# Kernel optimization log

Measured on AMD Instinct MI355X. Metric: run time of the kernel, lower is better.

## Reference

```python
import jax, jax.numpy as jnp
import numpy as np

B, S, DM = 2, 2048, 2048
H, DH = 16, 128
EPS = 1e-6


def rmsnorm(t, w):
    # normalize over last dim (head_dim), fp32 math
    var = jnp.mean(jnp.square(t), axis=-1, keepdims=True)
    return t * jax.lax.rsqrt(var + EPS) * w


def apply_rope(t, freqs):
    # t: (B,S,H,D); freqs: (S,1,D/2,2,2)
    b, s, h, d = t.shape
    t2 = t.reshape(b, s, h, 2, d // 2)
    t2 = jnp.moveaxis(t2, -2, -1)[..., None, :]  # (B,S,H,D/2,1,2)
    out = freqs[..., 0] * t2[..., 0] + freqs[..., 1] * t2[..., 1]  # (B,S,H,D/2,2)
    out = jnp.moveaxis(out, -1, -2).reshape(b, s, h, d)
    return out.astype(t.dtype)


def setup_inputs() -> dict:
    key = jax.random.key(0)
    ks = jax.random.split(key, 6)
    sc = 0.02
    return {
        "x": jax.random.normal(ks[0], (B, S, DM), jnp.float32),
        "rope_emb": jax.random.normal(ks[1], (S, 1, DH // 2, 2, 2), jnp.float32),
        "wq": jax.random.normal(ks[2], (DM, DM), jnp.float32) * sc,
        "wk": jax.random.normal(ks[3], (DM, DM), jnp.float32) * sc,
        "wv": jax.random.normal(ks[4], (DM, DM), jnp.float32) * sc,
        "wo": jax.random.normal(ks[5], (DM, DM), jnp.float32) * sc,
        "q_norm_w": jnp.ones((DH,), jnp.float32),
        "k_norm_w": jnp.ones((DH,), jnp.float32),
    }


def reference(x, rope_emb, wq, wk, wv, wo, q_norm_w, k_norm_w):
    b, s, _ = x.shape
    q = (x @ wq.T).reshape(b, s, H, DH)
    k = (x @ wk.T).reshape(b, s, H, DH)
    v = (x @ wv.T).reshape(b, s, H, DH)
    q = rmsnorm(q, q_norm_w)
    k = rmsnorm(k, k_norm_w)
    q = apply_rope(q, rope_emb)
    k = apply_rope(k, rope_emb)
    scale = 1.0 / np.sqrt(DH).astype(np.float32)
    scores = jnp.einsum('bqhd,bkhd->bhqk', q, k) * scale
    attn = jax.nn.softmax(scores, axis=-1)
    out = jnp.einsum('bhqk,bkhd->bqhd', attn, v).reshape(b, s, H * DH)
    return out @ wo.T
```

## Files before the change

kernel.cpp:

```cpp
#include <hip/hip_runtime.h>

typedef __bf16 bf16x8 __attribute__((ext_vector_type(8)));
typedef __bf16 bf16x4 __attribute__((ext_vector_type(4)));
typedef float floatx4 __attribute__((ext_vector_type(4)));

#define GK 2048
#define S_LEN 2048
#define NH 16
#define DH 128
#define NKT (GK / 64)

__device__ __forceinline__ void gl2lds16c(const __bf16* g, char* l) {
    __builtin_amdgcn_global_load_lds(
        (const __attribute__((address_space(1))) void*)g,
        (__attribute__((address_space(3))) void*)l, 16, 0, 0);
}

__global__ __launch_bounds__(256) void cvt_bf16(const float* __restrict__ in,
                                                __bf16* __restrict__ out, int n4) {
    int i = blockIdx.x * 256 + threadIdx.x;
    if (i < n4) {
        const float4 v = ((const float4*)in)[i];
        bf16x4 h;
        h[0] = (__bf16)v.x; h[1] = (__bf16)v.y; h[2] = (__bf16)v.z; h[3] = (__bf16)v.w;
        ((bf16x4*)out)[i] = h;
    }
}

__global__ __launch_bounds__(256) void cvt3_bf16(const float* __restrict__ a,
                                                 const float* __restrict__ b,
                                                 const float* __restrict__ c,
                                                 __bf16* __restrict__ out) {
    const int per = 2048 * 2048 / 4;
    int i = blockIdx.x * 256 + threadIdx.x;
    const float* src = a; int j = i;
    if (i >= 2 * per)      { src = c; j = i - 2 * per; }
    else if (i >= per)     { src = b; j = i - per; }
    const float4 v = ((const float4*)src)[j];
    bf16x4 h;
    h[0] = (__bf16)v.x; h[1] = (__bf16)v.y; h[2] = (__bf16)v.z; h[3] = (__bf16)v.w;
    ((bf16x4*)out)[i] = h;
}

__device__ __forceinline__ int xcd_remap(int L, int nwg) {
    return (L & 7) * (nwg >> 3) + (L >> 3);
}

__device__ __forceinline__ void gemm_body3(const __bf16* __restrict__ A,
                                           const __bf16* __restrict__ W,
                                           int m0, int n0, char* lds,
                                           floatx4 (*acc)[4]) {
    const int t = threadIdx.x, l = t & 63, wave = t >> 6;
    const int fr = l & 15, fq = l >> 4;
    const int wm = wave >> 2, wn = wave & 3;

    const int swcol = ((l & 7) * 8) ^ (((l >> 3) & 7) * 8);
    const __bf16* gA = A + (size_t)(m0 + wave * 8 + (l >> 3)) * GK + swcol;
    const __bf16* gW = W + (size_t)(n0 + wave * 8 + (l >> 3)) * GK + swcol;
    char* const ldsW = lds + wave * 1024;

    auto stageA = [&](int p, int kt, int q) {
        gl2lds16c(gA + (size_t)q * 64 * GK + kt * 64,
                  ldsW + p * 65536 + q * 8192);
    };
    auto stageBh = [&](int p, int kt, int h) {
        gl2lds16c(gW + (size_t)h * 64 * GK + kt * 64,
                  ldsW + p * 65536 + 32768 + h * 8192);
    };

#pragma unroll
    for (int q = 0; q < 4; q++) stageA(0, 0, q);
#pragma unroll
    for (int h = 0; h < 4; h++) stageBh(0, 0, h);
#pragma unroll
    for (int q = 0; q < 4; q++) stageA(1, 1, q);
#pragma unroll
    for (int h = 0; h < 4; h++) stageBh(1, 1, h);

    const int sw = (fr & 7) << 4;
    const int cb0 = (fq * 16) ^ sw;
    const int cb1 = (64 + fq * 16) ^ sw;

    for (int t0 = 0; t0 < NKT; t0++) {
        const int p = t0 & 1;
        if (t0 == NKT - 1) { asm volatile("s_waitcnt vmcnt(0)" ::: "memory"); }
        else               { asm volatile("s_waitcnt vmcnt(8)" ::: "memory"); }
        __builtin_amdgcn_s_barrier();
        asm volatile("" ::: "memory");

        const char* bufA = lds + p * 65536;
        const char* bufB = bufA + 32768;

        bf16x8 bB[4][2];
#pragma unroll
        for (int j = 0; j < 4; j++) {
            const char* rb = bufB + (wn * 64 + j * 16 + fr) * 128;
            bB[j][0] = *(const bf16x8*)(rb + cb0);
            bB[j][1] = *(const bf16x8*)(rb + cb1);
        }

#pragma unroll
        for (int q = 0; q < 4; q++) {
            if (t0 + 2 < NKT) {
                if (q == 1) { stageA(p, t0 + 2, 0); stageBh(p, t0 + 2, 0); stageBh(p, t0 + 2, 1); }
                if (q == 2) { stageA(p, t0 + 2, 1); stageBh(p, t0 + 2, 2); stageBh(p, t0 + 2, 3); }
                if (q == 3) { stageA(p, t0 + 2, 2); }
            }
            const char* ra = bufA + (q * 64 + wm * 32 + fr) * 128;
            bf16x8 bA[2][2];
#pragma unroll
            for (int i = 0; i < 2; i++) {
                bA[i][0] = *(const bf16x8*)(ra + i * 2048 + cb0);
                bA[i][1] = *(const bf16x8*)(ra + i * 2048 + cb1);
            }
            __builtin_amdgcn_s_setprio(1);
#pragma unroll
            for (int i = 0; i < 2; i++)
#pragma unroll
                for (int j = 0; j < 4; j++) {
                    acc[2 * q + i][j] = __builtin_amdgcn_mfma_f32_16x16x32_bf16(bA[i][0], bB[j][0], acc[2 * q + i][j], 0, 0, 0);
                    acc[2 * q + i][j] = __builtin_amdgcn_mfma_f32_16x16x32_bf16(bA[i][1], bB[j][1], acc[2 * q + i][j], 0, 0, 0);
                }
            __builtin_amdgcn_s_setprio(0);
            __builtin_amdgcn_s_barrier();
            asm volatile("" ::: "memory");
        }
        if (t0 + 2 < NKT) stageA(p, t0 + 2, 3);
    }
}

__global__ __launch_bounds__(512, 2) void gemm_qkv(const __bf16* __restrict__ A,
                                                   const __bf16* __restrict__ W,
                                                   __bf16* __restrict__ qb,
                                                   __bf16* __restrict__ kb,
                                                   __bf16* __restrict__ vbT) {
    extern __shared__ __align__(16) char lds[];
    const int gx = gridDim.x;
    const int L = blockIdx.x + gx * blockIdx.y;
    const int tid2 = xcd_remap(L, gx * (int)gridDim.y);
    const int m0 = (tid2 / gx) * 256, n0 = (tid2 % gx) * 256;
    floatx4 acc[8][4] = {};
    gemm_body3(A, W, m0, n0, lds, acc);

    const int lane = threadIdx.x & 63, wave = threadIdx.x >> 6;
    const int fr = lane & 15, fq = lane >> 4;
    const int wm = wave >> 2, wn = wave & 3;
    const int which = n0 >> 11;
    const int nc0 = n0 & 2047;

    for (int mi = 0; mi < 8; mi++)
        for (int j = 0; j < 4; j++) {
            const int row = m0 + (mi >> 1) * 64 + wm * 32 + (mi & 1) * 16 + fq * 4;
            const int col = nc0 + wn * 64 + j * 16 + fr;
            if (which == 2) {
                __bf16* Cp = vbT + (((size_t)(row & ~2047)) << 11) +
                             (size_t)col * 2048 + (row & 2047);
                bf16x4 hv;
                for (int r = 0; r < 4; r++) hv[r] = (__bf16)acc[mi][j][r];
                *(bf16x4*)Cp = hv;
            } else {
                __bf16* dst = which ? kb : qb;
                for (int r = 0; r < 4; r++)
                    dst[(size_t)(row + r) * 2048 + col] = (__bf16)acc[mi][j][r];
            }
        }
}

__global__ __launch_bounds__(512, 2) void gemm_out(const __bf16* __restrict__ A,
                                                   const __bf16* __restrict__ W,
                                                   float* __restrict__ C) {
    extern __shared__ __align__(16) char lds[];
    const int gx = gridDim.x;
    const int L = blockIdx.x + gx * blockIdx.y;
    const int tid2 = xcd_remap(L, gx * (int)gridDim.y);
    const int m0 = (tid2 / gx) * 256, n0 = (tid2 % gx) * 256;
    floatx4 acc[8][4] = {};
    gemm_body3(A, W, m0, n0, lds, acc);

    const int lane = threadIdx.x & 63, wave = threadIdx.x >> 6;
    const int fr = lane & 15, fq = lane >> 4;
    const int wm = wave >> 2, wn = wave & 3;
    for (int mi = 0; mi < 8; mi++)
        for (int j = 0; j < 4; j++) {
            const int row = m0 + (mi >> 1) * 64 + wm * 32 + (mi & 1) * 16 + fq * 4;
            const int col = n0 + wn * 64 + j * 16 + fr;
            for (int r = 0; r < 4; r++)
                C[(size_t)(row + r) * 2048 + col] = acc[mi][j][r];
        }
}

__global__ __launch_bounds__(256) void rmsrope(__bf16* __restrict__ qb,
                                               __bf16* __restrict__ kb,
                                               const float* __restrict__ rope,
                                               const float* __restrict__ qw,
                                               const float* __restrict__ kw) {
    const int lane = threadIdx.x & 63;
    const int row = blockIdx.x * 4 + (threadIdx.x >> 6);
    __bf16* p = (blockIdx.y ? kb : qb) + (size_t)row * DH;
    const float* w = blockIdx.y ? kw : qw;
    const int s = (row >> 4) & (S_LEN - 1);

    float t0 = (float)p[lane];
    float t1 = (float)p[lane + 64];
    float ss = t0 * t0 + t1 * t1;
    for (int o = 32; o; o >>= 1) ss += __shfl_xor(ss, o, 64);
    const float inv = rsqrtf(ss * (1.0f / 128.0f) + 1e-6f);
    t0 *= inv * w[lane];
    t1 *= inv * w[lane + 64];

    const float4 f = *(const float4*)(rope + (size_t)s * 256 + lane * 4);
    p[lane]      = (__bf16)(f.x * t0 + f.y * t1);
    p[lane + 64] = (__bf16)(f.z * t0 + f.w * t1);
}

__global__ __launch_bounds__(256) void flash(const __bf16* __restrict__ Q,
                                             const __bf16* __restrict__ K,
                                             const __bf16* __restrict__ Vt_g,
                                             __bf16* __restrict__ O) {
    __shared__ __align__(16) __bf16 Ks[32][136];
    __shared__ __align__(16) __bf16 Vt[144][40];
    __shared__ __align__(16) __bf16 Ps[4][32][40];

    const int t = threadIdx.x, lane = t & 63, wave = t >> 6;
    const int fr = lane & 15, fq = lane >> 4;

    const int n = blockIdx.x + (int)gridDim.x * blockIdx.y;
    const int by = (n & 7) * 4 + (n >> 7);
    const int bx = (n >> 3) & 15;
    const int b = by >> 4, h = by & 15;

    const size_t baseQ = (size_t)b * S_LEN * 2048 + h * 128;
    const size_t baseV = (size_t)b * 2048 * 2048 + (size_t)h * 128 * 2048;
    const int q0 = bx * 128 + wave * 32;
    const float sc2 = 0.08838834764831845f * 1.4426950408889634f;
    const float M2 = 12.0f * 1.4426950408889634f;

    for (int idx = t; idx < 16 * 40; idx += 256) {
        const int rr = idx / 40, cc = idx - rr * 40;
        Vt[128 + rr][cc] = (rr == 0) ? (__bf16)1.0f : (__bf16)0.0f;
    }

    bf16x8 qf[2][4];
    for (int i2 = 0; i2 < 2; i2++) {
        const __bf16* qp = Q + baseQ + (size_t)(q0 + i2 * 16 + fr) * 2048 + fq * 8;
        for (int c = 0; c < 4; c++) qf[i2][c] = *(const bf16x8*)(qp + c * 32);
    }

    floatx4 oa[2][9] = {};

    const __bf16* Kp = K + baseQ + (size_t)(t >> 3) * 2048 + (t & 7) * 16;
    const __bf16* Vp = Vt_g + baseV + (size_t)(t >> 1) * 2048 + (t & 1) * 16;

    for (int kv0 = 0; kv0 < S_LEN; kv0 += 32) {
        *(uint4*)&Ks[t >> 3][(t & 7) * 16]     = *(const uint4*)(Kp);
        *(uint4*)&Ks[t >> 3][(t & 7) * 16 + 8] = *(const uint4*)(Kp + 8);
        *(uint4*)&Vt[t >> 1][(t & 1) * 16]     = *(const uint4*)(Vp);
        *(uint4*)&Vt[t >> 1][(t & 1) * 16 + 8] = *(const uint4*)(Vp + 8);
        Kp += (size_t)32 * 2048;
        Vp += 32;
        __syncthreads();

        floatx4 sacc[2][2] = {};
        __builtin_amdgcn_s_setprio(1);
        for (int c = 0; c < 4; c++) {
            const bf16x8 kf0 = *(const bf16x8*)&Ks[fr][c * 32 + fq * 8];
            const bf16x8 kf1 = *(const bf16x8*)&Ks[fr + 16][c * 32 + fq * 8];
            sacc[0][0] = __builtin_amdgcn_mfma_f32_16x16x32_bf16(qf[0][c], kf0, sacc[0][0], 0, 0, 0);
            sacc[0][1] = __builtin_amdgcn_mfma_f32_16x16x32_bf16(qf[0][c], kf1, sacc[0][1], 0, 0, 0);
            sacc[1][0] = __builtin_amdgcn_mfma_f32_16x16x32_bf16(qf[1][c], kf0, sacc[1][0], 0, 0, 0);
            sacc[1][1] = __builtin_amdgcn_mfma_f32_16x16x32_bf16(qf[1][c], kf1, sacc[1][1], 0, 0, 0);
        }
        __builtin_amdgcn_s_setprio(0);

        for (int i2 = 0; i2 < 2; i2++)
            for (int r = 0; r < 4; r++) {
                const int row = i2 * 16 + fq * 4 + r;
                Ps[wave][row][fr]      = (__bf16)exp2f(fmaf(sc2, sacc[i2][0][r], -M2));
                Ps[wave][row][fr + 16] = (__bf16)exp2f(fmaf(sc2, sacc[i2][1][r], -M2));
            }

        const bf16x8 pf0 = *(const bf16x8*)&Ps[wave][fr][fq * 8];
        const bf16x8 pf1 = *(const bf16x8*)&Ps[wave][16 + fr][fq * 8];
        __builtin_amdgcn_s_setprio(1);
        for (int nb = 0; nb < 9; nb++) {
            const bf16x8 vf = *(const bf16x8*)&Vt[nb * 16 + fr][fq * 8];
            oa[0][nb] = __builtin_amdgcn_mfma_f32_16x16x32_bf16(pf0, vf, oa[0][nb], 0, 0, 0);
            oa[1][nb] = __builtin_amdgcn_mfma_f32_16x16x32_bf16(pf1, vf, oa[1][nb], 0, 0, 0);
        }
        __builtin_amdgcn_s_setprio(0);
        __syncthreads();
    }

    for (int i2 = 0; i2 < 2; i2++)
        for (int r = 0; r < 4; r++) {
            float l = oa[i2][8][r];
            l = __shfl(l, fq * 16);
            const float inv = 1.0f / l;
            __bf16* op = O + baseQ + (size_t)(q0 + i2 * 16 + fq * 4 + r) * 2048;
            for (int nb = 0; nb < 8; nb++)
                op[nb * 16 + fr] = (__bf16)(oa[i2][nb][r] * inv);
        }
}

extern "C" void kernel_launch(void* const* d_in, const int* in_sizes, int n_in,
                              void* d_out, int out_size, void* d_ws, size_t ws_size,
                              hipStream_t stream) {
    const float* x    = (const float*)d_in[0];
    const float* rope = (const float*)d_in[1];
    const float* wq   = (const float*)d_in[2];
    const float* wk   = (const float*)d_in[3];
    const float* wv   = (const float*)d_in[4];
    const float* wo   = (const float*)d_in[5];
    const float* qnw  = (const float*)d_in[6];
    const float* knw  = (const float*)d_in[7];
    float* out = (float*)d_out;

    static bool attr_set = false;
    if (!attr_set) {
        hipFuncSetAttribute((const void*)gemm_qkv,
                            hipFuncAttributeMaxDynamicSharedMemorySize, 131072);
        hipFuncSetAttribute((const void*)gemm_out,
                            hipFuncAttributeMaxDynamicSharedMemorySize, 131072);
        attr_set = true;
    }

    const size_t NTOK = 2 * 2048;
    const size_t ELEMS = NTOK * 2048;
    __bf16* xb  = (__bf16*)d_ws;
    __bf16* qb  = xb + ELEMS;
    __bf16* kb  = qb + ELEMS;
    __bf16* vbT = kb + ELEMS;
    __bf16* ob  = xb;
    __bf16* wqkv = (__bf16*)d_out;
    __bf16* wob  = qb;

    cvt_bf16<<<(int)(ELEMS / 4) / 256, 256, 0, stream>>>(x, xb, (int)(ELEMS / 4));
    cvt3_bf16<<<3 * (2048 * 2048 / 4) / 256, 256, 0, stream>>>(wq, wk, wv, wqkv);
    gemm_qkv<<<dim3(6144 / 256, (unsigned)(NTOK / 256)), 512, 131072, stream>>>(xb, wqkv, qb, kb, vbT);
    rmsrope<<<dim3((unsigned)(NTOK * 16 / 4), 2), 256, 0, stream>>>(qb, kb, rope, qnw, knw);
    flash<<<dim3(S_LEN / 128, 2 * 16), 256, 0, stream>>>(qb, kb, vbT, ob);
    cvt_bf16<<<(int)(2048 * 2048 / 4) / 256, 256, 0, stream>>>(wo, wob, 2048 * 2048 / 4);
    gemm_out<<<dim3(2048 / 256, (unsigned)(NTOK / 256)), 512, 131072, stream>>>(ob, wob, out);
}
```

Baseline: 445.4 us.

## Double-buffer flash K/V tiles via async global-to-LDS loads with swizzled layout

Rewrites the flash attention inner loop to process 64-key tiles, staged two iterations ahead with direct global-to-LDS loads into double-buffered dynamic shared memory. LDS layouts use XOR swizzles in place of padding to avoid bank conflicts, and the row-sum column comes from MFMAs against a register ones vector instead of an extra LDS V row. The goal is to overlap K/V fetch latency with compute and cut per-iteration barriers. The cost is 80KB of LDS per block, which limits occupancy, plus manual vmcnt bookkeeping that must stay correct.

```diff
diff --git a/kernel.cpp b/kernel.cpp
--- a/kernel.cpp
+++ b/kernel.cpp
@@ -213,13 +213,11 @@
     p[lane + 64] = (__bf16)(f.z * t0 + f.w * t1);
 }
 
-__global__ __launch_bounds__(256) void flash(const __bf16* __restrict__ Q,
-                                             const __bf16* __restrict__ K,
-                                             const __bf16* __restrict__ Vt_g,
-                                             __bf16* __restrict__ O) {
-    __shared__ __align__(16) __bf16 Ks[32][136];
-    __shared__ __align__(16) __bf16 Vt[144][40];
-    __shared__ __align__(16) __bf16 Ps[4][32][40];
+__global__ __launch_bounds__(256, 2) void flash(const __bf16* __restrict__ Q,
+                                                const __bf16* __restrict__ K,
+                                                const __bf16* __restrict__ Vt_g,
+                                                __bf16* __restrict__ O) {
+    extern __shared__ __align__(16) char lds[];
 
     const int t = threadIdx.x, lane = t & 63, wave = t >> 6;
     const int fr = lane & 15, fq = lane >> 4;
@@ -235,67 +233,127 @@
     const float sc2 = 0.08838834764831845f * 1.4426950408889634f;
     const float M2 = 12.0f * 1.4426950408889634f;
 
-    for (int idx = t; idx < 16 * 40; idx += 256) {
-        const int rr = idx / 40, cc = idx - rr * 40;
-        Vt[128 + rr][cc] = (rr == 0) ? (__bf16)1.0f : (__bf16)0.0f;
-    }
-
     bf16x8 qf[2][4];
+#pragma unroll
     for (int i2 = 0; i2 < 2; i2++) {
         const __bf16* qp = Q + baseQ + (size_t)(q0 + i2 * 16 + fr) * 2048 + fq * 8;
+#pragma unroll
         for (int c = 0; c < 4; c++) qf[i2][c] = *(const bf16x8*)(qp + c * 32);
     }
+    asm volatile("s_waitcnt vmcnt(0)" ::: "memory");
+
+    bf16x8 onesb;
+#pragma unroll
+    for (int e = 0; e < 8; e++) onesb[e] = (__bf16)1.0f;
+
+    const int l4 = lane >> 4;
+    const int c16 = lane & 15;
+    const int l3 = lane >> 3;
+    const int c8 = lane & 7;
+    const __bf16* gK0 = K + baseQ + (size_t)(wave * 16 + l4) * 2048 + (c16 ^ l4) * 8;
+    const __bf16* gK1 = K + baseQ + (size_t)(wave * 16 + l4) * 2048 + (c16 ^ (4 + l4)) * 8;
+    const __bf16* gV  = Vt_g + baseV + (size_t)(wave * 8 + l3) * 2048 + (c8 ^ l3) * 8;
+
+    char* const kdw = lds + wave * 4096;
+    char* const vdw = lds + 32768 + wave * 1024;
+
+    auto stage = [&](int p, int it2) {
+        const size_t ko = (size_t)it2 * 64 * 2048;
+        char* kd = kdw + p * 16384;
+        gl2lds16c(gK0 + ko,                      kd);
+        gl2lds16c(gK1 + ko + (size_t)4 * 2048,   kd + 1024);
+        gl2lds16c(gK0 + ko + (size_t)8 * 2048,   kd + 2048);
+        gl2lds16c(gK1 + ko + (size_t)12 * 2048,  kd + 3072);
+        const __bf16* v = gV + it2 * 64;
+        char* vd = vdw + p * 16384;
+        gl2lds16c(v,                        vd);
+        gl2lds16c(v + (size_t)32 * 2048,    vd + 4096);
+        gl2lds16c(v + (size_t)64 * 2048,    vd + 8192);
+        gl2lds16c(v + (size_t)96 * 2048,    vd + 12288);
+    };
+
+    stage(0, 0);
+    stage(1, 1);
 
     floatx4 oa[2][9] = {};
-
-    const __bf16* Kp = K + baseQ + (size_t)(t >> 3) * 2048 + (t & 7) * 16;
-    const __bf16* Vp = Vt_g + baseV + (size_t)(t >> 1) * 2048 + (t & 1) * 16;
-
-    for (int kv0 = 0; kv0 < S_LEN; kv0 += 32) {
-        *(uint4*)&Ks[t >> 3][(t & 7) * 16]     = *(const uint4*)(Kp);
-        *(uint4*)&Ks[t >> 3][(t & 7) * 16 + 8] = *(const uint4*)(Kp + 8);
-        *(uint4*)&Vt[t >> 1][(t & 1) * 16]     = *(const uint4*)(Vp);
-        *(uint4*)&Vt[t >> 1][(t & 1) * 16 + 8] = *(const uint4*)(Vp + 8);
-        Kp += (size_t)32 * 2048;
-        Vp += 32;
-        __syncthreads();
-
-        floatx4 sacc[2][2] = {};
-        __builtin_amdgcn_s_setprio(1);
-        for (int c = 0; c < 4; c++) {
-            const bf16x8 kf0 = *(const bf16x8*)&Ks[fr][c * 32 + fq * 8];
-            const bf16x8 kf1 = *(const bf16x8*)&Ks[fr + 16][c * 32 + fq * 8];
-            sacc[0][0] = __builtin_amdgcn_mfma_f32_16x16x32_bf16(qf[0][c], kf0, sacc[0][0], 0, 0, 0);
-            sacc[0][1] = __builtin_amdgcn_mfma_f32_16x16x32_bf16(qf[0][c], kf1, sacc[0][1], 0, 0, 0);
-            sacc[1][0] = __builtin_amdgcn_mfma_f32_16x16x32_bf16(qf[1][c], kf0, sacc[1][0], 0, 0, 0);
-            sacc[1][1] = __builtin_amdgcn_mfma_f32_16x16x32_bf16(qf[1][c], kf1, sacc[1][1], 0, 0, 0);
-        }
-        __builtin_amdgcn_s_setprio(0);
-
+    char* const Pw = lds + 65536 + wave * 4096;
+    const int sw = (fr & 7) << 4;
+
+    for (int it = 0; it < 32; ++it) {
+        const int p = it & 1;
+        if (it == 31) { asm volatile("s_waitcnt vmcnt(0)" ::: "memory"); }
+        else          { asm volatile("s_waitcnt vmcnt(8)" ::: "memory"); }
+        __builtin_amdgcn_s_barrier();
+        asm volatile("" ::: "memory");
+
+        const char* Kb = lds + p * 16384;
+        const char* Vb = lds + 32768 + p * 16384;
+
+        floatx4 sacc[2][4] = {};
+#pragma unroll
+        for (int j = 0; j < 4; j++) {
+            const char* kr = Kb + (j * 16 + fr) * 256;
+            const bf16x8 kf0 = *(const bf16x8*)(kr + ((0 + fq * 16) ^ sw));
+            const bf16x8 kf1 = *(const bf16x8*)(kr + ((64 + fq * 16) ^ sw));
+            const bf16x8 kf2 = *(const bf16x8*)(kr + ((128 + fq * 16) ^ sw));
+            const bf16x8 kf3 = *(const bf16x8*)(kr + ((192 + fq * 16) ^ sw));
+            __builtin_amdgcn_s_setprio(1);
+            sacc[0][j] = __builtin_amdgcn_mfma_f32_16x16x32_bf16(qf[0][0], kf0, sacc[0][j], 0, 0, 0);
+            sacc[1][j] = __builtin_amdgcn_mfma_f32_16x16x32_bf16(qf[1][0], kf0, sacc[1][j], 0, 0, 0);
+            sacc[0][j] = __builtin_amdgcn_mfma_f32_16x16x32_bf16(qf[0][1], kf1, sacc[0][j], 0, 0, 0);
+            sacc[1][j] = __builtin_amdgcn_mfma_f32_16x16x32_bf16(qf[1][1], kf1, sacc[1][j], 0, 0, 0);
+            sacc[0][j] = __builtin_amdgcn_mfma_f32_16x16x32_bf16(qf[0][2], kf2, sacc[0][j], 0, 0, 0);
+            sacc[1][j] = __builtin_amdgcn_mfma_f32_16x16x32_bf16(qf[1][2], kf2, sacc[1][j], 0, 0, 0);
+            sacc[0][j] = __builtin_amdgcn_mfma_f32_16x16x32_bf16(qf[0][3], kf3, sacc[0][j], 0, 0, 0);
+            sacc[1][j] = __builtin_amdgcn_mfma_f32_16x16x32_bf16(qf[1][3], kf3, sacc[1][j], 0, 0, 0);
+            __builtin_amdgcn_s_setprio(0);
+        }
+
+#pragma unroll
         for (int i2 = 0; i2 < 2; i2++)
+#pragma unroll
             for (int r = 0; r < 4; r++) {
                 const int row = i2 * 16 + fq * 4 + r;
-                Ps[wave][row][fr]      = (__bf16)exp2f(fmaf(sc2, sacc[i2][0][r], -M2));
-                Ps[wave][row][fr + 16] = (__bf16)exp2f(fmaf(sc2, sacc[i2][1][r], -M2));
+                char* pr = Pw + row * 128;
+                const int rsw = ((fq * 4 + r) & 7) << 4;
+#pragma unroll
+                for (int j = 0; j < 4; j++)
+                    *(__bf16*)(pr + ((j * 32 + fr * 2) ^ rsw)) =
+                        (__bf16)exp2f(fmaf(sc2, sacc[i2][j][r], -M2));
             }
 
-        const bf16x8 pf0 = *(const bf16x8*)&Ps[wave][fr][fq * 8];
-        const bf16x8 pf1 = *(const bf16x8*)&Ps[wave][16 + fr][fq * 8];
-        __builtin_amdgcn_s_setprio(1);
-        for (int nb = 0; nb < 9; nb++) {
-            const bf16x8 vf = *(const bf16x8*)&Vt[nb * 16 + fr][fq * 8];
-            oa[0][nb] = __builtin_amdgcn_mfma_f32_16x16x32_bf16(pf0, vf, oa[0][nb], 0, 0, 0);
-            oa[1][nb] = __builtin_amdgcn_mfma_f32_16x16x32_bf16(pf1, vf, oa[1][nb], 0, 0, 0);
-        }
-        __builtin_amdgcn_s_setprio(0);
-        __syncthreads();
+        bf16x8 pf[2][2];
+#pragma unroll
+        for (int i2 = 0; i2 < 2; i2++) {
+            const char* pr = Pw + (i2 * 16 + fr) * 128;
+            pf[i2][0] = *(const bf16x8*)(pr + ((fq * 16) ^ sw));
+            pf[i2][1] = *(const bf16x8*)(pr + ((64 + fq * 16) ^ sw));
+        }
+#pragma unroll
+        for (int nb = 0; nb < 8; nb++) {
+            const char* vr = Vb + (nb * 16 + fr) * 128;
+            const bf16x8 vf0 = *(const bf16x8*)(vr + ((fq * 16) ^ sw));
+            const bf16x8 vf1 = *(const bf16x8*)(vr + ((64 + fq * 16) ^ sw));
+            __builtin_amdgcn_s_setprio(1);
+            oa[0][nb] = __builtin_amdgcn_mfma_f32_16x16x32_bf16(pf[0][0], vf0, oa[0][nb], 0, 0, 0);
+            oa[1][nb] = __builtin_amdgcn_mfma_f32_16x16x32_bf16(pf[1][0], vf0, oa[1][nb], 0, 0, 0);
+            oa[0][nb] = __builtin_amdgcn_mfma_f32_16x16x32_bf16(pf[0][1], vf1, oa[0][nb], 0, 0, 0);
+            oa[1][nb] = __builtin_amdgcn_mfma_f32_16x16x32_bf16(pf[1][1], vf1, oa[1][nb], 0, 0, 0);
+            __builtin_amdgcn_s_setprio(0);
+        }
+        oa[0][8] = __builtin_amdgcn_mfma_f32_16x16x32_bf16(pf[0][0], onesb, oa[0][8], 0, 0, 0);
+        oa[1][8] = __builtin_amdgcn_mfma_f32_16x16x32_bf16(pf[1][0], onesb, oa[1][8], 0, 0, 0);
+        oa[0][8] = __builtin_amdgcn_mfma_f32_16x16x32_bf16(pf[0][1], onesb, oa[0][8], 0, 0, 0);
+        oa[1][8] = __builtin_amdgcn_mfma_f32_16x16x32_bf16(pf[1][1], onesb, oa[1][8], 0, 0, 0);
+
+        __builtin_amdgcn_s_barrier();
+        asm volatile("" ::: "memory");
+        if (it < 30) stage(p, it + 2);
     }
 
     for (int i2 = 0; i2 < 2; i2++)
         for (int r = 0; r < 4; r++) {
-            float l = oa[i2][8][r];
-            l = __shfl(l, fq * 16);
-            const float inv = 1.0f / l;
+            const float inv = 1.0f / oa[i2][8][r];
             __bf16* op = O + baseQ + (size_t)(q0 + i2 * 16 + fq * 4 + r) * 2048;
             for (int nb = 0; nb < 8; nb++)
                 op[nb * 16 + fr] = (__bf16)(oa[i2][nb][r] * inv);
@@ -321,6 +379,8 @@
                             hipFuncAttributeMaxDynamicSharedMemorySize, 131072);
         hipFuncSetAttribute((const void*)gemm_out,
                             hipFuncAttributeMaxDynamicSharedMemorySize, 131072);
+        hipFuncSetAttribute((const void*)flash,
+                            hipFuncAttributeMaxDynamicSharedMemorySize, 81920);
         attr_set = true;
     }
 
@@ -338,7 +398,7 @@
     cvt3_bf16<<<3 * (2048 * 2048 / 4) / 256, 256, 0, stream>>>(wq, wk, wv, wqkv);
     gemm_qkv<<<dim3(6144 / 256, (unsigned)(NTOK / 256)), 512, 131072, stream>>>(xb, wqkv, qb, kb, vbT);
     rmsrope<<<dim3((unsigned)(NTOK * 16 / 4), 2), 256, 0, stream>>>(qb, kb, rope, qnw, knw);
-    flash<<<dim3(S_LEN / 128, 2 * 16), 256, 0, stream>>>(qb, kb, vbT, ob);
+    flash<<<dim3(S_LEN / 128, 2 * 16), 256, 81920, stream>>>(qb, kb, vbT, ob);
     cvt_bf16<<<(int)(2048 * 2048 / 4) / 256, 256, 0, stream>>>(wo, wob, 2048 * 2048 / 4);
     gemm_out<<<dim3(2048 / 256, (unsigned)(NTOK / 256)), 512, 131072, stream>>>(ob, wob, out);
 }
```

New measurement: 411.2 us. -7.7%, faster.
